# Performance work log

Hardware: AMD Instinct MI355X
Metric: run time of the kernel (lower is better)

## Reference

```python
import jax, jax.numpy as jnp
import numpy as np

nT, nB, H, V = 256, 256, 1024, 32000

def setup_inputs() -> dict:
    key = jax.random.key(0)
    ks = jax.random.split(key, 16)
    s = 0.02
    return {
        "tokens": jax.random.randint(ks[0], (nB,), 0, V),
        "prev_hidden": jax.random.normal(ks[1], (1, nB, H), dtype=jnp.float32),
        "enc_outputs": jax.random.normal(ks[2], (nT, nB, H), dtype=jnp.float32),
        "emb": jax.random.normal(ks[3], (V, H), dtype=jnp.float32) * s,
        "W_i2h": jax.random.normal(ks[4], (H, H), dtype=jnp.float32) * s,
        "W_h2h": jax.random.normal(ks[5], (H, H), dtype=jnp.float32) * s,
        "b_h2h": jnp.zeros((H,), dtype=jnp.float32),
        "w_score": jax.random.normal(ks[6], (H,), dtype=jnp.float32) * s,
        "W_ih": jax.random.normal(ks[7], (3 * H, 2 * H), dtype=jnp.float32) * s,
        "b_ih": jnp.zeros((3 * H,), dtype=jnp.float32),
        "W_hh": jax.random.normal(ks[8], (3 * H, H), dtype=jnp.float32) * s,
        "b_hh": jnp.zeros((3 * H,), dtype=jnp.float32),
        "W_out": jax.random.normal(ks[9], (V, H), dtype=jnp.float32) * s,
        "b_out": jnp.zeros((V,), dtype=jnp.float32),
    }

def reference(tokens, prev_hidden, enc_outputs, emb, W_i2h, W_h2h, b_h2h,
              w_score, W_ih, b_ih, W_hh, b_hh, W_out, b_out):
    h0 = prev_hidden[0]                                     # [nB,H]
    cur_emb = emb[tokens]                                   # [nB,H] (dropout = identity at inference)
    # additive (Bahdanau) attention energies
    enc_proj = jnp.einsum('tbh,oh->tbo', enc_outputs, W_i2h)  # [nT,nB,H]
    h_proj = h0 @ W_h2h.T + b_h2h                           # [nB,H]
    e = jnp.einsum('tbh,h->tb', jnp.tanh(enc_proj + h_proj[None]), w_score)  # [nT,nB]
    alpha = jax.nn.softmax(e.T, axis=1)                     # [nB,nT], softmax over time
    context = jnp.einsum('bt,tbh->bh', alpha, enc_outputs)  # [nB,H]
    x = jnp.concatenate([context, cur_emb], axis=1)         # [nB,2H]
    # single GRU step (PyTorch gate order: r, z, n)
    gi = x @ W_ih.T + b_ih                                  # [nB,3H]
    gh = h0 @ W_hh.T + b_hh                                 # [nB,3H]
    hs = h0.shape[-1]
    r = jax.nn.sigmoid(gi[:, :hs] + gh[:, :hs])
    z = jax.nn.sigmoid(gi[:, hs:2*hs] + gh[:, hs:2*hs])
    n = jnp.tanh(gi[:, 2*hs:] + r * gh[:, 2*hs:])
    h_new = (1.0 - z) * n + z * h0                          # [nB,H]
    out = jax.nn.log_softmax(h_new @ W_out.T + b_out, axis=1)  # [nB,V]
    return out, h_new[None], alpha
```

## Files before the change

### kernel.cpp

```cpp
#include <hip/hip_runtime.h>
#include <hip/hip_bf16.h>

typedef __attribute__((ext_vector_type(8))) short bf16x8;
typedef __attribute__((ext_vector_type(4))) float f32x4;
typedef __attribute__((ext_vector_type(4))) int i32x4;
typedef __attribute__((ext_vector_type(4))) unsigned short u16x4;
typedef __attribute__((ext_vector_type(8))) unsigned short u16x8;

#define LDS_STRIDE 72

__device__ __forceinline__ unsigned short f2bf(float f) {
    __hip_bfloat16 h = __float2bfloat16(f);
    unsigned short u; __builtin_memcpy(&u, &h, 2); return u;
}
__device__ __forceinline__ float bf2f(unsigned short u) {
    union { unsigned u; float f; } v; v.u = ((unsigned)u) << 16; return v.f;
}
__device__ __forceinline__ float fast_sigmoid(float x) { return 1.f / (1.f + __expf(-x)); }
__device__ __forceinline__ float fast_tanh(float x)    { return 1.f - 2.f / (__expf(2.f * x) + 1.f); }

#define GLOAD_LDS16(gp, lp) __builtin_amdgcn_global_load_lds( \
    (const __attribute__((address_space(1))) void*)(gp), \
    (__attribute__((address_space(3))) void*)(lp), 16, 0, 0)


#define STA(LB, HF, PTR) do { \
    GLOAD_LDS16((PTR), &AL[LB][HF][ldsrow][0]); \
    GLOAD_LDS16((PTR) + 65536, &AL[LB][HF][64 + ldsrow][0]); \
} while (0)

#define STB(LB, HF, PTR) do { \
    GLOAD_LDS16((PTR), &BL[LB][HF][ldsrow][0]); \
    GLOAD_LDS16((PTR) + 65536, &BL[LB][HF][64 + ldsrow][0]); \
} while (0)

#define LDA(DST, BUF, MH, KS) do { \
    const int c_ = ((KS)*32 + fg*8) ^ swzr; \
    _Pragma("unroll") \
    for (int mi = 0; mi < 4; ++mi) \
        DST[mi] = *(const bf16x8*)&AL[BUF][wr][(MH)*64 + mi*16 + fr][c_]; \
} while (0)

#define LDB(DST, BUF, KS) do { \
    const int c_ = ((KS)*32 + fg*8) ^ swzr; \
    _Pragma("unroll") \
    for (int ni = 0; ni < 4; ++ni) \
        DST[ni] = *(const bf16x8*)&BL[BUF][bh][br0 + ni*16 + fr][c_]; \
} while (0)

#define MM(AV, BV, MH) do { \
    _Pragma("unroll") \
    for (int mi = 0; mi < 4; ++mi) \
        _Pragma("unroll") \
        for (int ni = 0; ni < 4; ++ni) \
            acc[(MH)*4 + mi][ni] = __builtin_amdgcn_mfma_f32_16x16x32_bf16( \
                AV[mi], BV[ni], acc[(MH)*4 + mi][ni], 0, 0, 0); \
} while (0)

#define SP1 __builtin_amdgcn_s_setprio(1)
#define SP0 __builtin_amdgcn_s_setprio(0)
#define BAR asm volatile("s_barrier" ::: "memory")
#define VMC8 asm volatile("s_waitcnt vmcnt(8)" ::: "memory")
#define VMC0 asm volatile("s_waitcnt vmcnt(0)" ::: "memory")

__global__ __launch_bounds__(512, 1)
void gemm8p_e(const unsigned short* __restrict__ Ag, const unsigned short* __restrict__ Bg,
              const float* __restrict__ hproj, const float* __restrict__ wscore,
              float* __restrict__ epart)
{
    const int tid = threadIdx.x;
    const int lane = tid & 63, wid = tid >> 6;
    const int fr = lane & 15, fg = lane >> 4;
    const int wr = wid >> 2;
    const int wc = wid & 3;
    const int bh = wc >> 1, br0 = (wc & 1) * 64;

    const int cpx = (int)gridDim.x >> 3;
    const int swz = ((int)blockIdx.x & 7) * cpx + ((int)blockIdx.x >> 3);
    const int mb = swz >> 2, nb = swz & 3;
    const int m0 = mb << 8, n0 = nb << 8;

    __shared__ unsigned short AL[3][2][128][64];
    __shared__ unsigned short BL[2][2][128][64];

    const int srow = lane >> 3;
    const int scol = ((lane & 7) ^ srow) << 3;
    const int swzr = (fr & 7) << 3;
    const int ldsrow = wid * 8;

    const unsigned short* pA0 = Ag + (size_t)(m0 + ldsrow + srow) * 1024 + scol;
    const unsigned short* pA1 = pA0 + (size_t)128 * 1024;
    const unsigned short* pB0 = Bg + (size_t)(n0 + ldsrow + srow) * 1024 + scol;
    const unsigned short* pB1 = pB0 + (size_t)128 * 1024;

    f32x4 acc[8][4];
#pragma unroll
    for (int i = 0; i < 8; ++i)
#pragma unroll
        for (int j = 0; j < 4; ++j) acc[i][j] = (f32x4){0.f, 0.f, 0.f, 0.f};
    bf16x8 avA[4], avB[4], bvA[4], bvB[4];

    STA(0, 0, pA0);      STA(0, 1, pA1);
    STB(0, 0, pB0);      STB(0, 1, pB1);
    STA(1, 0, pA0 + 64); STA(1, 1, pA1 + 64);
    STB(1, 0, pB0 + 64); STB(1, 1, pB1 + 64);
    VMC8;
    BAR;

#pragma unroll
    for (int t = 0; t < 16; t += 2) {
        const int tof = t * 64;
        const int a0 = t % 3, a1 = (t + 1) % 3, a2 = (t + 2) % 3, a3 = (t + 3) % 3;
        LDB(bvA, 0, 0); LDA(avA, a0, 0, 0);
        SP1; MM(avA, bvA, 0); SP0;
        LDB(bvB, 0, 1); LDA(avB, a0, 0, 1);
        if (t + 2 < 16) STA(a2, 0, pA0 + tof + 128);
        BAR;
        SP1; MM(avB, bvB, 0); SP0;
        LDA(avA, a0, 1, 0);
        if (t + 2 < 16) STA(a2, 1, pA1 + tof + 128);
        BAR;
        SP1; MM(avA, bvA, 1); SP0;
        LDA(avB, a0, 1, 1);
        if (t + 2 < 16) STB(0, 0, pB0 + tof + 128);
        BAR;
        SP1; MM(avB, bvB, 1); SP0;
        if (t + 2 < 16) { STB(0, 1, pB1 + tof + 128); VMC8; } else { VMC0; }
        BAR;
        LDB(bvA, 1, 0); LDA(avA, a1, 0, 0);
        SP1; MM(avA, bvA, 0); SP0;
        LDB(bvB, 1, 1); LDA(avB, a1, 0, 1);
        if (t + 3 < 16) STA(a3, 0, pA0 + tof + 192);
        BAR;
        SP1; MM(avB, bvB, 0); SP0;
        LDA(avA, a1, 1, 0);
        if (t + 3 < 16) STA(a3, 1, pA1 + tof + 192);
        BAR;
        SP1; MM(avA, bvA, 1); SP0;
        LDA(avB, a1, 1, 1);
        if (t + 3 < 16) STB(1, 0, pB0 + tof + 192);
        BAR;
        SP1; MM(avB, bvB, 1); SP0;
        if (t + 3 < 16) { STB(1, 1, pB1 + tof + 192); VMC8; }
        BAR;
    }

    float wsv[4];
#pragma unroll
    for (int ni = 0; ni < 4; ++ni) wsv[ni] = wscore[n0 + wc * 64 + ni * 16 + fr];
#pragma unroll
    for (int mi = 0; mi < 8; ++mi)
#pragma unroll
        for (int r = 0; r < 4; ++r) {
            const int bb = wr * 128 + mi * 16 + fg * 4 + r;
            const float* hp = hproj + (size_t)bb * 1024 + n0 + wc * 64 + fr;
            float s = 0.f;
#pragma unroll
            for (int ni = 0; ni < 4; ++ni)
                s += fast_tanh(acc[mi][ni][r] + hp[ni * 16]) * wsv[ni];
            s += __shfl_xor(s, 1); s += __shfl_xor(s, 2);
            s += __shfl_xor(s, 4); s += __shfl_xor(s, 8);
            if (fr == 0) epart[((size_t)bb * 256 + mb) * 16 + nb * 4 + wc] = s;
        }
}

__global__ __launch_bounds__(256, 2)
void gemm_h2(const float* __restrict__ h0,
             const float* __restrict__ Wh2h, const float* __restrict__ Whh,
             const float* __restrict__ bh2h, const float* __restrict__ bhh,
             float* __restrict__ hproj, float* __restrict__ gh)
{
    const int mb = blockIdx.x & 1;
    const int nbg = blockIdx.x >> 1;
    const float* Bf; const float* bias; float* Cout; int Nst; int n0;
    if (nbg < 8) { Bf = Wh2h; bias = bh2h; Cout = hproj; Nst = 1024; n0 = nbg << 7; }
    else         { Bf = Whh;  bias = bhh;  Cout = gh;    Nst = 3072; n0 = (nbg - 8) << 7; }

    const int m0 = mb << 7;
    const int tid = threadIdx.x;
    const int lane = tid & 63, wid = tid >> 6;
    const int fr = lane & 15, fg = lane >> 4;
    const int srow = tid >> 1, shalf = (tid & 1) * 32;

    extern __shared__ char smem[];
    typedef unsigned short (*tile_t)[128][LDS_STRIDE];
    tile_t As = (tile_t)smem;
    tile_t Bs = (tile_t)(smem + 2 * 128 * LDS_STRIDE * 2);

    f32x4 acc[2][8];
#pragma unroll
    for (int i = 0; i < 2; ++i)
#pragma unroll
        for (int j = 0; j < 8; ++j) acc[i][j] = (f32x4){0.f, 0.f, 0.f, 0.f};

    float a_f[32], b_f[32];

    auto loadA = [&](int kt) {
        size_t base = (size_t)(m0 + srow) * 1024 + (size_t)kt * 64 + shalf;
#pragma unroll
        for (int j = 0; j < 8; ++j) *(f32x4*)&a_f[j * 4] = *(const f32x4*)(h0 + base + j * 4);
    };
    auto loadB = [&](int kt) {
        size_t base = (size_t)(n0 + srow) * 1024 + (size_t)kt * 64 + shalf;
#pragma unroll
        for (int j = 0; j < 8; ++j) *(f32x4*)&b_f[j * 4] = *(const f32x4*)(Bf + base + j * 4);
    };
    auto storeA = [&](int buf) {
        unsigned short t[32];
#pragma unroll
        for (int j = 0; j < 32; ++j) t[j] = f2bf(a_f[j]);
#pragma unroll
        for (int j = 0; j < 4; ++j) *(i32x4*)&As[buf][srow][shalf + j * 8] = *(i32x4*)&t[j * 8];
    };
    auto storeB = [&](int buf) {
        unsigned short t[32];
#pragma unroll
        for (int j = 0; j < 32; ++j) t[j] = f2bf(b_f[j]);
#pragma unroll
        for (int j = 0; j < 4; ++j) *(i32x4*)&Bs[buf][srow][shalf + j * 8] = *(i32x4*)&t[j * 8];
    };

    loadA(0); loadB(0);
    storeA(0); storeB(0);
    __syncthreads();

    for (int kt = 0; kt < 16; ++kt) {
        const int cur = kt & 1;
        if (kt + 1 < 16) { loadA(kt + 1); loadB(kt + 1); }
#pragma unroll
        for (int ks = 0; ks < 2; ++ks) {
            bf16x8 av[2], bv[8];
#pragma unroll
            for (int mi = 0; mi < 2; ++mi)
                av[mi] = *(const bf16x8*)&As[cur][wid * 32 + mi * 16 + fr][ks * 32 + fg * 8];
#pragma unroll
            for (int ni = 0; ni < 8; ++ni)
                bv[ni] = *(const bf16x8*)&Bs[cur][ni * 16 + fr][ks * 32 + fg * 8];
#pragma unroll
            for (int mi = 0; mi < 2; ++mi)
#pragma unroll
                for (int ni = 0; ni < 8; ++ni)
                    acc[mi][ni] = __builtin_amdgcn_mfma_f32_16x16x32_bf16(av[mi], bv[ni], acc[mi][ni], 0, 0, 0);
        }
        if (kt + 1 < 16) { storeA(cur ^ 1); storeB(cur ^ 1); }
        __syncthreads();
    }

#pragma unroll
    for (int mi = 0; mi < 2; ++mi)
#pragma unroll
        for (int r = 0; r < 4; ++r) {
            const int m = m0 + wid * 32 + mi * 16 + fg * 4 + r;
#pragma unroll
            for (int ni = 0; ni < 8; ++ni) {
                const int col = n0 + ni * 16 + fr;
                Cout[(size_t)m * Nst + col] = acc[mi][ni][r] + bias[col];
            }
        }
}

template<int EPI, bool ABF, bool BBF>
__global__ __launch_bounds__(256, 2)
void gemm_rs(const void* __restrict__ Agv, const void* __restrict__ Bgv,
             const float* __restrict__ bias, float* __restrict__ Cout,
             unsigned short* __restrict__ CoutB,
             const float* __restrict__ hproj, const float* __restrict__ wscore,
             float* __restrict__ epart, float* __restrict__ lsepart,
             int M, int N, int K)
{
    const int nbn = N >> 7;
    const int nmb = M >> 7;
    int mb, nb;
    if (EPI == 1) {
        int cpx = gridDim.x >> 3;
        int bp = (blockIdx.x & 7) * cpx + (blockIdx.x >> 3);
        mb = bp / nbn; nb = bp % nbn;
    } else {
        mb = blockIdx.x % nmb; nb = blockIdx.x / nmb;
    }
    const int m0 = mb << 7, n0 = nb << 7;
    const int tid = threadIdx.x;
    const int lane = tid & 63, wid = tid >> 6;
    const int fr = lane & 15, fg = lane >> 4;
    const int srow = tid >> 1, shalf = (tid & 1) * 32;

    extern __shared__ char smem[];
    typedef unsigned short (*tile_t)[128][LDS_STRIDE];
    tile_t As = (tile_t)smem;
    tile_t Bs = (tile_t)(smem + 2 * 128 * LDS_STRIDE * 2);

    const float* Af = (const float*)Agv;
    const unsigned short* Ab = (const unsigned short*)Agv;
    const float* Bf = (const float*)Bgv;
    const unsigned short* Bb = (const unsigned short*)Bgv;

    f32x4 acc[2][8];
#pragma unroll
    for (int i = 0; i < 2; ++i)
#pragma unroll
        for (int j = 0; j < 8; ++j) acc[i][j] = (f32x4){0.f, 0.f, 0.f, 0.f};

    float a_f[32]; unsigned short a_b[32];
    float b_f[32]; unsigned short b_b[32];

    auto loadA = [&](int kt) {
        size_t base = (size_t)(m0 + srow) * K + (size_t)kt * 64 + shalf;
        if (ABF) {
#pragma unroll
            for (int j = 0; j < 4; ++j) *(i32x4*)&a_b[j * 8] = *(const i32x4*)(Ab + base + j * 8);
        } else {
#pragma unroll
            for (int j = 0; j < 8; ++j) *(f32x4*)&a_f[j * 4] = *(const f32x4*)(Af + base + j * 4);
        }
    };
    auto loadB = [&](int kt) {
        size_t base = (size_t)(n0 + srow) * K + (size_t)kt * 64 + shalf;
        if (BBF) {
#pragma unroll
            for (int j = 0; j < 4; ++j) *(i32x4*)&b_b[j * 8] = *(const i32x4*)(Bb + base + j * 8);
        } else {
#pragma unroll
            for (int j = 0; j < 8; ++j) *(f32x4*)&b_f[j * 4] = *(const f32x4*)(Bf + base + j * 4);
        }
    };
    auto storeA = [&](int buf) {
        unsigned short tA[32];
        if (ABF) {
#pragma unroll
            for (int j = 0; j < 32; ++j) tA[j] = a_b[j];
        } else {
#pragma unroll
            for (int j = 0; j < 32; ++j) tA[j] = f2bf(a_f[j]);
        }
#pragma unroll
        for (int j = 0; j < 4; ++j) *(i32x4*)&As[buf][srow][shalf + j * 8] = *(i32x4*)&tA[j * 8];
    };
    auto storeB = [&](int buf) {
        unsigned short tB[32];
        if (BBF) {
#pragma unroll
            for (int j = 0; j < 32; ++j) tB[j] = b_b[j];
        } else {
#pragma unroll
            for (int j = 0; j < 32; ++j) tB[j] = f2bf(b_f[j]);
        }
#pragma unroll
        for (int j = 0; j < 4; ++j) *(i32x4*)&Bs[buf][srow][shalf + j * 8] = *(i32x4*)&tB[j * 8];
    };

    const int nkt = K >> 6;

    loadA(0); loadB(0);
    storeA(0); storeB(0);
    __syncthreads();

    for (int kt = 0; kt < nkt; ++kt) {
        const int cur = kt & 1;
        if (kt + 1 < nkt) { loadA(kt + 1); loadB(kt + 1); }
#pragma unroll
        for (int ks = 0; ks < 2; ++ks) {
            bf16x8 av[2], bv[8];
#pragma unroll
            for (int mi = 0; mi < 2; ++mi)
                av[mi] = *(const bf16x8*)&As[cur][wid * 32 + mi * 16 + fr][ks * 32 + fg * 8];
#pragma unroll
            for (int ni = 0; ni < 8; ++ni)
                bv[ni] = *(const bf16x8*)&Bs[cur][ni * 16 + fr][ks * 32 + fg * 8];
#pragma unroll
            for (int mi = 0; mi < 2; ++mi)
#pragma unroll
                for (int ni = 0; ni < 8; ++ni)
                    acc[mi][ni] = __builtin_amdgcn_mfma_f32_16x16x32_bf16(av[mi], bv[ni], acc[mi][ni], 0, 0, 0);
        }
        if (kt + 1 < nkt) { storeA(cur ^ 1); storeB(cur ^ 1); }
        __syncthreads();
    }

    if (EPI == 0) {
#pragma unroll
        for (int mi = 0; mi < 2; ++mi)
#pragma unroll
            for (int r = 0; r < 4; ++r) {
                const int m = m0 + wid * 32 + mi * 16 + fg * 4 + r;
#pragma unroll
                for (int ni = 0; ni < 8; ++ni) {
                    const int col = n0 + ni * 16 + fr;
                    Cout[(size_t)m * N + col] = acc[mi][ni][r] + bias[col];
                }
            }
    } else if (EPI == 1) {
        float wsv[8];
#pragma unroll
        for (int ni = 0; ni < 8; ++ni) wsv[ni] = wscore[n0 + ni * 16 + fr];
#pragma unroll
        for (int mi = 0; mi < 2; ++mi)
#pragma unroll
            for (int r = 0; r < 4; ++r) {
                const int m = m0 + wid * 32 + mi * 16 + fg * 4 + r;
                const int bb = m & 255, tt = m >> 8;
                const float* hp = hproj + (size_t)bb * 1024 + n0 + fr;
                float s = 0.f;
#pragma unroll
                for (int ni = 0; ni < 8; ++ni)
                    s += fast_tanh(acc[mi][ni][r] + hp[ni * 16]) * wsv[ni];
                s += __shfl_xor(s, 1); s += __shfl_xor(s, 2);
                s += __shfl_xor(s, 4); s += __shfl_xor(s, 8);
                if (fr == 0) epart[((size_t)bb * 256 + tt) * 8 + nb] = s;
            }
    } else {
#pragma unroll
        for (int mi = 0; mi < 2; ++mi)
#pragma unroll
            for (int r = 0; r < 4; ++r) {
                const int m = m0 + wid * 32 + mi * 16 + fg * 4 + r;
                float vv[8];
                float mx = -3.4e38f;
#pragma unroll
                for (int ni = 0; ni < 8; ++ni) {
                    const int col = n0 + ni * 16 + fr;
                    vv[ni] = acc[mi][ni][r] + bias[col];
                    CoutB[(size_t)m * N + col] = f2bf(vv[ni]);
                    mx = fmaxf(mx, vv[ni]);
                }
                mx = fmaxf(mx, __shfl_xor(mx, 1));
                mx = fmaxf(mx, __shfl_xor(mx, 2));
                mx = fmaxf(mx, __shfl_xor(mx, 4));
                mx = fmaxf(mx, __shfl_xor(mx, 8));
                float se = 0.f;
#pragma unroll
                for (int ni = 0; ni < 8; ++ni) se += __expf(vv[ni] - mx);
                se += __shfl_xor(se, 1); se += __shfl_xor(se, 2);
                se += __shfl_xor(se, 4); se += __shfl_xor(se, 8);
                if (fr == 0) {
                    lsepart[((size_t)m * nbn + nb) * 2]     = mx;
                    lsepart[((size_t)m * nbn + nb) * 2 + 1] = se;
                }
            }
    }
}

__global__ void prep_all(const float* __restrict__ enc, unsigned short* __restrict__ encB,
                         const float* __restrict__ Wi2h, unsigned short* __restrict__ WiB,
                         const float* __restrict__ emb, const int* __restrict__ tokens,
                         unsigned short* __restrict__ xB)
{
    const int ENC4 = 16777216, WI4 = 262144, EMB4 = 65536;
    const int total = ENC4 + WI4 + EMB4;
    for (int i = blockIdx.x * 256 + threadIdx.x; i < total; i += gridDim.x * 256) {
        f32x4 v; unsigned short* dst;
        if (i < ENC4) {
            v = *(const f32x4*)(enc + (size_t)i * 4);
            dst = encB + (size_t)i * 4;
        } else if (i < ENC4 + WI4) {
            int j = i - ENC4;
            v = *(const f32x4*)(Wi2h + (size_t)j * 4);
            dst = WiB + (size_t)j * 4;
        } else {
            int j = i - ENC4 - WI4;
            int b = j >> 8, h4 = j & 255;
            v = *(const f32x4*)(emb + (size_t)tokens[b] * 1024 + h4 * 4);
            dst = xB + (size_t)b * 2048 + 1024 + h4 * 4;
        }
        u16x4 o;
#pragma unroll
        for (int j = 0; j < 4; ++j) o[j] = f2bf(v[j]);
        *(u16x4*)dst = o;
    }
}

__global__ void prep_kernel(const float* __restrict__ Wi2h, unsigned short* __restrict__ WiB,
                            const float* __restrict__ emb, const int* __restrict__ tokens,
                            unsigned short* __restrict__ xB)
{
    int i = blockIdx.x * 256 + threadIdx.x;
    if (i < 262144) {
        f32x4 v = *(const f32x4*)(Wi2h + (size_t)i * 4);
        u16x4 o;
#pragma unroll
        for (int j = 0; j < 4; ++j) o[j] = f2bf(v[j]);
        *(u16x4*)(WiB + (size_t)i * 4) = o;
    } else {
        int j = i - 262144;
        int b = j >> 8, h4 = j & 255;
        int tok = tokens[b];
        f32x4 v = *(const f32x4*)(emb + (size_t)tok * 1024 + h4 * 4);
        u16x4 o;
#pragma unroll
        for (int jj = 0; jj < 4; ++jj) o[jj] = f2bf(v[jj]);
        *(u16x4*)(xB + (size_t)b * 2048 + 1024 + h4 * 4) = o;
    }
}

__global__ __launch_bounds__(256) void softmax_alpha(const float* __restrict__ epart,
                                                     float* __restrict__ alpha, int pw)
{
    const int b = blockIdx.x, t = threadIdx.x;
    const int lane = t & 63, w = t >> 6;
    const float* ep = epart + ((size_t)b * 256 + t) * pw;
    float s = 0.f;
    for (int j = 0; j < pw; ++j) s += ep[j];
    __shared__ float rmax[4], rsum[4];
    float mx = s;
#pragma unroll
    for (int d = 1; d < 64; d <<= 1) mx = fmaxf(mx, __shfl_xor(mx, d));
    if (lane == 0) rmax[w] = mx;
    __syncthreads();
    mx = fmaxf(fmaxf(rmax[0], rmax[1]), fmaxf(rmax[2], rmax[3]));
    float p = __expf(s - mx);
    float sm = p;
#pragma unroll
    for (int d = 1; d < 64; d <<= 1) sm += __shfl_xor(sm, d);
    if (lane == 0) rsum[w] = sm;
    __syncthreads();
    sm = rsum[0] + rsum[1] + rsum[2] + rsum[3];
    alpha[(size_t)b * 256 + t] = p / sm;
}

__global__ __launch_bounds__(128) void ctx_part_bf(const float* __restrict__ alpha,
                                                   const unsigned short* __restrict__ encB,
                                                   float* __restrict__ pc)
{
    const int b = blockIdx.x, tc = blockIdx.y;
    const int h8 = threadIdx.x;
    const float* al = alpha + (size_t)b * 256 + tc * 64;
    float acc[8];
#pragma unroll
    for (int j = 0; j < 8; ++j) acc[j] = 0.f;
#pragma unroll 4
    for (int i = 0; i < 64; ++i) {
        float a = al[i];
        u16x8 e = *(const u16x8*)(encB + ((size_t)(tc * 64 + i) * 256 + b) * 1024 + h8 * 8);
#pragma unroll
        for (int j = 0; j < 8; ++j) acc[j] += bf2f(e[j]) * a;
    }
    float* d = pc + ((size_t)tc * 256 + b) * 1024 + h8 * 8;
    *(f32x4*)d = *(f32x4*)&acc[0];
    *(f32x4*)(d + 4) = *(f32x4*)&acc[4];
}

__global__ __launch_bounds__(256) void ctx_part(const float* __restrict__ alpha,
                                                const float* __restrict__ enc,
                                                float* __restrict__ pc)
{
    const int b = blockIdx.x, tc = blockIdx.y;
    const int h4 = threadIdx.x;
    const float* al = alpha + (size_t)b * 256 + tc * 64;
    f32x4 acc = {0.f, 0.f, 0.f, 0.f};
#pragma unroll 4
    for (int i = 0; i < 64; ++i) {
        float a = al[i];
        f32x4 e = *(const f32x4*)(enc + ((size_t)(tc * 64 + i) * 256 + b) * 1024 + h4 * 4);
        acc += e * a;
    }
    *(f32x4*)(pc + ((size_t)tc * 256 + b) * 1024 + h4 * 4) = acc;
}

__global__ void ctx_fin(const float* __restrict__ pc, unsigned short* __restrict__ xB)
{
    const int b = blockIdx.x, h4 = threadIdx.x;
    f32x4 c = {0.f, 0.f, 0.f, 0.f};
#pragma unroll
    for (int tc = 0; tc < 4; ++tc)
        c += *(const f32x4*)(pc + ((size_t)tc * 256 + b) * 1024 + h4 * 4);
    u16x4 o;
#pragma unroll
    for (int j = 0; j < 4; ++j) o[j] = f2bf(c[j]);
    *(u16x4*)(xB + (size_t)b * 2048 + h4 * 4) = o;
}

__global__ void gru_kernel(const float* __restrict__ gi, const float* __restrict__ gh,
                           const float* __restrict__ h0, float* __restrict__ hnew,
                           unsigned short* __restrict__ hnB)
{
    int idx = blockIdx.x * 256 + threadIdx.x;
    int b = idx >> 10, h = idx & 1023;
    size_t gb = (size_t)b * 3072;
    float r = fast_sigmoid(gi[gb + h]        + gh[gb + h]);
    float z = fast_sigmoid(gi[gb + 1024 + h] + gh[gb + 1024 + h]);
    float n = fast_tanh   (gi[gb + 2048 + h] + r * gh[gb + 2048 + h]);
    float hp = h0[idx];
    float hn = (1.f - z) * n + z * hp;
    hnew[idx] = hn;
    hnB[idx] = f2bf(hn);
}

__global__ void lse_reduce(const float* __restrict__ lsepart, float* __restrict__ lse, int nbn)
{
    const int m = blockIdx.x, l = threadIdx.x;
    float mx = -3.4e38f, s = 0.f;
    for (int p = l; p < nbn; p += 64) {
        float pm = lsepart[((size_t)m * nbn + p) * 2];
        float ps = lsepart[((size_t)m * nbn + p) * 2 + 1];
        float nm = fmaxf(mx, pm);
        s = s * __expf(mx - nm) + ps * __expf(pm - nm);
        mx = nm;
    }
#pragma unroll
    for (int d = 1; d < 64; d <<= 1) {
        float om = __shfl_xor(mx, d), os = __shfl_xor(s, d);
        float nm = fmaxf(mx, om);
        s = s * __expf(mx - nm) + os * __expf(om - nm);
        mx = nm;
    }
    if (l == 0) lse[m] = mx + __logf(s);
}

__global__ void lsub_bf(const unsigned short* __restrict__ lgB,
                        const float* __restrict__ lse, float* __restrict__ out)
{
    int f = blockIdx.x * 256 + threadIdx.x;
    float l = lse[f / 4000];
    u16x8 v = *(const u16x8*)(lgB + (size_t)f * 8);
    float* o = out + (size_t)f * 8;
    f32x4 o0, o1;
#pragma unroll
    for (int j = 0; j < 4; ++j) o0[j] = bf2f(v[j]) - l;
#pragma unroll
    for (int j = 0; j < 4; ++j) o1[j] = bf2f(v[4 + j]) - l;
    *(f32x4*)o = o0;
    *(f32x4*)(o + 4) = o1;
}

extern "C" void kernel_launch(void* const* d_in, const int* in_sizes, int n_in,
                              void* d_out, int out_size, void* d_ws, size_t ws_size,
                              hipStream_t stream)
{
    const int*   tokens  = (const int*)  d_in[0];
    const float* h0      = (const float*)d_in[1];
    const float* enc     = (const float*)d_in[2];
    const float* emb     = (const float*)d_in[3];
    const float* W_i2h   = (const float*)d_in[4];
    const float* W_h2h   = (const float*)d_in[5];
    const float* b_h2h   = (const float*)d_in[6];
    const float* w_score = (const float*)d_in[7];
    const float* W_ih    = (const float*)d_in[8];
    const float* b_ih    = (const float*)d_in[9];
    const float* W_hh    = (const float*)d_in[10];
    const float* b_hh    = (const float*)d_in[11];
    const float* W_out   = (const float*)d_in[12];
    const float* b_out   = (const float*)d_in[13];

    float* out   = (float*)d_out;
    float* hnew  = out + (size_t)256 * 32000;
    float* alpha = hnew + 256 * 1024;

    const size_t RS_LDS = 2u * 2u * 128u * LDS_STRIDE * 2u;

    char* w = (char*)d_ws;
    const size_t NEED = (size_t)153 * (1 << 20);

    if (ws_size >= NEED) {
        unsigned short* encB  = (unsigned short*)(w);
        unsigned short* lgB   = (unsigned short*)(w);
        unsigned short* WiB   = (unsigned short*)(w + (size_t)128 * (1 << 20));
        float* hproj          = (float*)(w + (size_t)130 * (1 << 20));
        float* gh             = (float*)(w + (size_t)131 * (1 << 20));
        float* epart          = (float*)(w + (size_t)134 * (1 << 20));
        float* pc             = (float*)(w + (size_t)138 * (1 << 20));
        unsigned short* xB    = (unsigned short*)(w + (size_t)142 * (1 << 20));
        float* gi             = (float*)(w + (size_t)143 * (1 << 20));
        unsigned short* hnB   = (unsigned short*)(w + (size_t)146 * (1 << 20));
        float* lsepart        = (float*)(w + (size_t)147 * (1 << 20));
        float* lse            = (float*)(w + (size_t)148 * (1 << 20));

        prep_all<<<2048, 256, 0, stream>>>(enc, encB, W_i2h, WiB, emb, tokens, xB);
        gemm_h2<<<64, 256, RS_LDS, stream>>>(h0, W_h2h, W_hh, b_h2h, b_hh, hproj, gh);
        gemm8p_e<<<1024, 512, 0, stream>>>(encB, WiB, hproj, w_score, epart);
        softmax_alpha<<<256, 256, 0, stream>>>(epart, alpha, 16);
        ctx_part_bf<<<dim3(256, 4), 128, 0, stream>>>(alpha, encB, pc);
        ctx_fin<<<256, 256, 0, stream>>>(pc, xB);
        gemm_rs<0, true, false><<<48, 256, RS_LDS, stream>>>(xB, W_ih, b_ih, gi,
            nullptr, nullptr, nullptr, nullptr, nullptr, 256, 3072, 2048);
        gru_kernel<<<1024, 256, 0, stream>>>(gi, gh, h0, hnew, hnB);
        gemm_rs<2, true, false><<<500, 256, RS_LDS, stream>>>(hnB, W_out, b_out, nullptr,
            lgB, nullptr, nullptr, nullptr, lsepart, 256, 32000, 1024);
        lse_reduce<<<256, 64, 0, stream>>>(lsepart, lse, 250);
        lsub_bf<<<4000, 256, 0, stream>>>(lgB, lse, out);
    } else {
        unsigned short* WiB   = (unsigned short*)(w);
        float* hproj          = (float*)(w + (size_t)2  * (1 << 20));
        float* gh             = (float*)(w + (size_t)3  * (1 << 20));
        float* epart          = (float*)(w + (size_t)6  * (1 << 20));
        float* pc             = (float*)(w + (size_t)8  * (1 << 20));
        unsigned short* xB    = (unsigned short*)(w + (size_t)12 * (1 << 20));
        float* gi             = (float*)(w + (size_t)13 * (1 << 20));
        unsigned short* hnB   = (unsigned short*)(w + (size_t)16 * (1 << 20));
        float* lsepart        = (float*)(w + (size_t)17 * (1 << 20));
        float* lse            = (float*)(w + (size_t)18 * (1 << 20));
        unsigned short* lgB   = (unsigned short*)(w + (size_t)19 * (1 << 20));

        prep_kernel<<<1280, 256, 0, stream>>>(W_i2h, WiB, emb, tokens, xB);
        gemm_h2<<<64, 256, RS_LDS, stream>>>(h0, W_h2h, W_hh, b_h2h, b_hh, hproj, gh);
        gemm_rs<1, false, true><<<4096, 256, RS_LDS, stream>>>(enc, WiB, nullptr, nullptr,
            nullptr, hproj, w_score, epart, nullptr, 65536, 1024, 1024);
        softmax_alpha<<<256, 256, 0, stream>>>(epart, alpha, 8);
        ctx_part<<<dim3(256, 4), 256, 0, stream>>>(alpha, enc, pc);
        ctx_fin<<<256, 256, 0, stream>>>(pc, xB);
        gemm_rs<0, true, false><<<48, 256, RS_LDS, stream>>>(xB, W_ih, b_ih, gi,
            nullptr, nullptr, nullptr, nullptr, nullptr, 256, 3072, 2048);
        gru_kernel<<<1024, 256, 0, stream>>>(gi, gh, h0, hnew, hnB);
        gemm_rs<2, true, false><<<500, 256, RS_LDS, stream>>>(hnB, W_out, b_out, nullptr,
            lgB, nullptr, nullptr, nullptr, lsepart, 256, 32000, 1024);
        lse_reduce<<<256, 64, 0, stream>>>(lsepart, lse, 250);
        lsub_bf<<<4000, 256, 0, stream>>>(lgB, lse, out);
    }
}
```

Baseline: 479.3 us.

## Merge prep with h2 GEMM, split-K gi GEMM, fuse LSE reduce and subtract

Folds the h0 projection GEMM into the prep conversion kernel as 64 extra blocks, so both run concurrently in one launch. Replaces the 48-block gi GEMM with a 4-way split-K version (192 blocks) whose partials are summed in a new GRU kernel together with the bias. Fuses the LSE reduction and the log-softmax subtraction into one kernel. The aim is to cut launch count and fill an underoccupied GEMM, at the cost of extra partial-sum traffic and a fused lse_sub kernel that uses only 256 blocks.

```diff
diff --git a/kernel.cpp b/kernel.cpp
--- a/kernel.cpp
+++ b/kernel.cpp
@@ -164,14 +164,13 @@
         }
 }
 
-__global__ __launch_bounds__(256, 2)
-void gemm_h2(const float* __restrict__ h0,
-             const float* __restrict__ Wh2h, const float* __restrict__ Whh,
-             const float* __restrict__ bh2h, const float* __restrict__ bhh,
-             float* __restrict__ hproj, float* __restrict__ gh)
-{
-    const int mb = blockIdx.x & 1;
-    const int nbg = blockIdx.x >> 1;
+__device__ void h2_body(char* smem, int blk, const float* __restrict__ h0,
+                        const float* __restrict__ Wh2h, const float* __restrict__ Whh,
+                        const float* __restrict__ bh2h, const float* __restrict__ bhh,
+                        float* __restrict__ hproj, float* __restrict__ gh)
+{
+    const int mb = blk & 1;
+    const int nbg = blk >> 1;
     const float* Bf; const float* bias; float* Cout; int Nst; int n0;
     if (nbg < 8) { Bf = Wh2h; bias = bh2h; Cout = hproj; Nst = 1024; n0 = nbg << 7; }
     else         { Bf = Whh;  bias = bhh;  Cout = gh;    Nst = 3072; n0 = (nbg - 8) << 7; }
@@ -182,7 +181,6 @@
     const int fr = lane & 15, fg = lane >> 4;
     const int srow = tid >> 1, shalf = (tid & 1) * 32;
 
-    extern __shared__ char smem[];
     typedef unsigned short (*tile_t)[128][LDS_STRIDE];
     tile_t As = (tile_t)smem;
     tile_t Bs = (tile_t)(smem + 2 * 128 * LDS_STRIDE * 2);
@@ -259,194 +257,25 @@
         }
 }
 
-template<int EPI, bool ABF, bool BBF>
 __global__ __launch_bounds__(256, 2)
-void gemm_rs(const void* __restrict__ Agv, const void* __restrict__ Bgv,
-             const float* __restrict__ bias, float* __restrict__ Cout,
-             unsigned short* __restrict__ CoutB,
-             const float* __restrict__ hproj, const float* __restrict__ wscore,
-             float* __restrict__ epart, float* __restrict__ lsepart,
-             int M, int N, int K)
-{
-    const int nbn = N >> 7;
-    const int nmb = M >> 7;
-    int mb, nb;
-    if (EPI == 1) {
-        int cpx = gridDim.x >> 3;
-        int bp = (blockIdx.x & 7) * cpx + (blockIdx.x >> 3);
-        mb = bp / nbn; nb = bp % nbn;
-    } else {
-        mb = blockIdx.x % nmb; nb = blockIdx.x / nmb;
-    }
-    const int m0 = mb << 7, n0 = nb << 7;
-    const int tid = threadIdx.x;
-    const int lane = tid & 63, wid = tid >> 6;
-    const int fr = lane & 15, fg = lane >> 4;
-    const int srow = tid >> 1, shalf = (tid & 1) * 32;
-
+void prep_h2(const float* __restrict__ enc, unsigned short* __restrict__ encB,
+             const float* __restrict__ Wi2h, unsigned short* __restrict__ WiB,
+             const float* __restrict__ emb, const int* __restrict__ tokens,
+             unsigned short* __restrict__ xB,
+             const float* __restrict__ h0,
+             const float* __restrict__ Wh2h, const float* __restrict__ Whh,
+             const float* __restrict__ bh2h, const float* __restrict__ bhh,
+             float* __restrict__ hproj, float* __restrict__ gh)
+{
     extern __shared__ char smem[];
-    typedef unsigned short (*tile_t)[128][LDS_STRIDE];
-    tile_t As = (tile_t)smem;
-    tile_t Bs = (tile_t)(smem + 2 * 128 * LDS_STRIDE * 2);
-
-    const float* Af = (const float*)Agv;
-    const unsigned short* Ab = (const unsigned short*)Agv;
-    const float* Bf = (const float*)Bgv;
-    const unsigned short* Bb = (const unsigned short*)Bgv;
-
-    f32x4 acc[2][8];
-#pragma unroll
-    for (int i = 0; i < 2; ++i)
-#pragma unroll
-        for (int j = 0; j < 8; ++j) acc[i][j] = (f32x4){0.f, 0.f, 0.f, 0.f};
-
-    float a_f[32]; unsigned short a_b[32];
-    float b_f[32]; unsigned short b_b[32];
-
-    auto loadA = [&](int kt) {
-        size_t base = (size_t)(m0 + srow) * K + (size_t)kt * 64 + shalf;
-        if (ABF) {
-#pragma unroll
-            for (int j = 0; j < 4; ++j) *(i32x4*)&a_b[j * 8] = *(const i32x4*)(Ab + base + j * 8);
-        } else {
-#pragma unroll
-            for (int j = 0; j < 8; ++j) *(f32x4*)&a_f[j * 4] = *(const f32x4*)(Af + base + j * 4);
-        }
-    };
-    auto loadB = [&](int kt) {
-        size_t base = (size_t)(n0 + srow) * K + (size_t)kt * 64 + shalf;
-        if (BBF) {
-#pragma unroll
-            for (int j = 0; j < 4; ++j) *(i32x4*)&b_b[j * 8] = *(const i32x4*)(Bb + base + j * 8);
-        } else {
-#pragma unroll
-            for (int j = 0; j < 8; ++j) *(f32x4*)&b_f[j * 4] = *(const f32x4*)(Bf + base + j * 4);
-        }
-    };
-    auto storeA = [&](int buf) {
-        unsigned short tA[32];
-        if (ABF) {
-#pragma unroll
-            for (int j = 0; j < 32; ++j) tA[j] = a_b[j];
-        } else {
-#pragma unroll
-            for (int j = 0; j < 32; ++j) tA[j] = f2bf(a_f[j]);
-        }
-#pragma unroll
-        for (int j = 0; j < 4; ++j) *(i32x4*)&As[buf][srow][shalf + j * 8] = *(i32x4*)&tA[j * 8];
-    };
-    auto storeB = [&](int buf) {
-        unsigned short tB[32];
-        if (BBF) {
-#pragma unroll
-            for (int j = 0; j < 32; ++j) tB[j] = b_b[j];
-        } else {
-#pragma unroll
-            for (int j = 0; j < 32; ++j) tB[j] = f2bf(b_f[j]);
-        }
-#pragma unroll
-        for (int j = 0; j < 4; ++j) *(i32x4*)&Bs[buf][srow][shalf + j * 8] = *(i32x4*)&tB[j * 8];
-    };
-
-    const int nkt = K >> 6;
-
-    loadA(0); loadB(0);
-    storeA(0); storeB(0);
-    __syncthreads();
-
-    for (int kt = 0; kt < nkt; ++kt) {
-        const int cur = kt & 1;
-        if (kt + 1 < nkt) { loadA(kt + 1); loadB(kt + 1); }
-#pragma unroll
-        for (int ks = 0; ks < 2; ++ks) {
-            bf16x8 av[2], bv[8];
-#pragma unroll
-            for (int mi = 0; mi < 2; ++mi)
-                av[mi] = *(const bf16x8*)&As[cur][wid * 32 + mi * 16 + fr][ks * 32 + fg * 8];
-#pragma unroll
-            for (int ni = 0; ni < 8; ++ni)
-                bv[ni] = *(const bf16x8*)&Bs[cur][ni * 16 + fr][ks * 32 + fg * 8];
-#pragma unroll
-            for (int mi = 0; mi < 2; ++mi)
-#pragma unroll
-                for (int ni = 0; ni < 8; ++ni)
-                    acc[mi][ni] = __builtin_amdgcn_mfma_f32_16x16x32_bf16(av[mi], bv[ni], acc[mi][ni], 0, 0, 0);
-        }
-        if (kt + 1 < nkt) { storeA(cur ^ 1); storeB(cur ^ 1); }
-        __syncthreads();
-    }
-
-    if (EPI == 0) {
-#pragma unroll
-        for (int mi = 0; mi < 2; ++mi)
-#pragma unroll
-            for (int r = 0; r < 4; ++r) {
-                const int m = m0 + wid * 32 + mi * 16 + fg * 4 + r;
-#pragma unroll
-                for (int ni = 0; ni < 8; ++ni) {
-                    const int col = n0 + ni * 16 + fr;
-                    Cout[(size_t)m * N + col] = acc[mi][ni][r] + bias[col];
-                }
-            }
-    } else if (EPI == 1) {
-        float wsv[8];
-#pragma unroll
-        for (int ni = 0; ni < 8; ++ni) wsv[ni] = wscore[n0 + ni * 16 + fr];
-#pragma unroll
-        for (int mi = 0; mi < 2; ++mi)
-#pragma unroll
-            for (int r = 0; r < 4; ++r) {
-                const int m = m0 + wid * 32 + mi * 16 + fg * 4 + r;
-                const int bb = m & 255, tt = m >> 8;
-                const float* hp = hproj + (size_t)bb * 1024 + n0 + fr;
-                float s = 0.f;
-#pragma unroll
-                for (int ni = 0; ni < 8; ++ni)
-                    s += fast_tanh(acc[mi][ni][r] + hp[ni * 16]) * wsv[ni];
-                s += __shfl_xor(s, 1); s += __shfl_xor(s, 2);
-                s += __shfl_xor(s, 4); s += __shfl_xor(s, 8);
-                if (fr == 0) epart[((size_t)bb * 256 + tt) * 8 + nb] = s;
-            }
-    } else {
-#pragma unroll
-        for (int mi = 0; mi < 2; ++mi)
-#pragma unroll
-            for (int r = 0; r < 4; ++r) {
-                const int m = m0 + wid * 32 + mi * 16 + fg * 4 + r;
-                float vv[8];
-                float mx = -3.4e38f;
-#pragma unroll
-                for (int ni = 0; ni < 8; ++ni) {
-                    const int col = n0 + ni * 16 + fr;
-                    vv[ni] = acc[mi][ni][r] + bias[col];
-                    CoutB[(size_t)m * N + col] = f2bf(vv[ni]);
-                    mx = fmaxf(mx, vv[ni]);
-                }
-                mx = fmaxf(mx, __shfl_xor(mx, 1));
-                mx = fmaxf(mx, __shfl_xor(mx, 2));
-                mx = fmaxf(mx, __shfl_xor(mx, 4));
-                mx = fmaxf(mx, __shfl_xor(mx, 8));
-                float se = 0.f;
-#pragma unroll
-                for (int ni = 0; ni < 8; ++ni) se += __expf(vv[ni] - mx);
-                se += __shfl_xor(se, 1); se += __shfl_xor(se, 2);
-                se += __shfl_xor(se, 4); se += __shfl_xor(se, 8);
-                if (fr == 0) {
-                    lsepart[((size_t)m * nbn + nb) * 2]     = mx;
-                    lsepart[((size_t)m * nbn + nb) * 2 + 1] = se;
-                }
-            }
-    }
-}
-
-__global__ void prep_all(const float* __restrict__ enc, unsigned short* __restrict__ encB,
-                         const float* __restrict__ Wi2h, unsigned short* __restrict__ WiB,
-                         const float* __restrict__ emb, const int* __restrict__ tokens,
-                         unsigned short* __restrict__ xB)
-{
+    if (blockIdx.x < 64) {
+        h2_body(smem, blockIdx.x, h0, Wh2h, Whh, bh2h, bhh, hproj, gh);
+        return;
+    }
     const int ENC4 = 16777216, WI4 = 262144, EMB4 = 65536;
     const int total = ENC4 + WI4 + EMB4;
-    for (int i = blockIdx.x * 256 + threadIdx.x; i < total; i += gridDim.x * 256) {
+    const int stride = ((int)gridDim.x - 64) * 256;
+    for (int i = ((int)blockIdx.x - 64) * 256 + (int)threadIdx.x; i < total; i += stride) {
         f32x4 v; unsigned short* dst;
         if (i < ENC4) {
             v = *(const f32x4*)(enc + (size_t)i * 4);
@@ -468,6 +297,285 @@
     }
 }
 
+__global__ __launch_bounds__(256, 2)
+void gemm_h2(const float* __restrict__ h0,
+             const float* __restrict__ Wh2h, const float* __restrict__ Whh,
+             const float* __restrict__ bh2h, const float* __restrict__ bhh,
+             float* __restrict__ hproj, float* __restrict__ gh)
+{
+    extern __shared__ char smem[];
+    h2_body(smem, blockIdx.x, h0, Wh2h, Whh, bh2h, bhh, hproj, gh);
+}
+
+__global__ __launch_bounds__(256, 2)
+void gemm_gi(const unsigned short* __restrict__ xB, const float* __restrict__ Wih,
+             float* __restrict__ gip)
+{
+    const int s = blockIdx.x / 48;
+    const int b = blockIdx.x % 48;
+    const int mb = b & 1, nb = b >> 1;
+    const int m0 = mb << 7, n0 = nb << 7;
+    const int kbase = s * 512;
+    const int tid = threadIdx.x;
+    const int lane = tid & 63, wid = tid >> 6;
+    const int fr = lane & 15, fg = lane >> 4;
+    const int srow = tid >> 1, shalf = (tid & 1) * 32;
+
+    extern __shared__ char smem[];
+    typedef unsigned short (*tile_t)[128][LDS_STRIDE];
+    tile_t As = (tile_t)smem;
+    tile_t Bs = (tile_t)(smem + 2 * 128 * LDS_STRIDE * 2);
+
+    f32x4 acc[2][8];
+#pragma unroll
+    for (int i = 0; i < 2; ++i)
+#pragma unroll
+        for (int j = 0; j < 8; ++j) acc[i][j] = (f32x4){0.f, 0.f, 0.f, 0.f};
+
+    unsigned short a_b[32]; float b_f[32];
+
+    auto loadA = [&](int kt) {
+        size_t base = (size_t)(m0 + srow) * 2048 + kbase + (size_t)kt * 64 + shalf;
+#pragma unroll
+        for (int j = 0; j < 4; ++j) *(i32x4*)&a_b[j * 8] = *(const i32x4*)(xB + base + j * 8);
+    };
+    auto loadB = [&](int kt) {
+        size_t base = (size_t)(n0 + srow) * 2048 + kbase + (size_t)kt * 64 + shalf;
+#pragma unroll
+        for (int j = 0; j < 8; ++j) *(f32x4*)&b_f[j * 4] = *(const f32x4*)(Wih + base + j * 4);
+    };
+    auto storeA = [&](int buf) {
+#pragma unroll
+        for (int j = 0; j < 4; ++j) *(i32x4*)&As[buf][srow][shalf + j * 8] = *(i32x4*)&a_b[j * 8];
+    };
+    auto storeB = [&](int buf) {
+        unsigned short t[32];
+#pragma unroll
+        for (int j = 0; j < 32; ++j) t[j] = f2bf(b_f[j]);
+#pragma unroll
+        for (int j = 0; j < 4; ++j) *(i32x4*)&Bs[buf][srow][shalf + j * 8] = *(i32x4*)&t[j * 8];
+    };
+
+    loadA(0); loadB(0);
+    storeA(0); storeB(0);
+    __syncthreads();
+
+    for (int kt = 0; kt < 8; ++kt) {
+        const int cur = kt & 1;
+        if (kt + 1 < 8) { loadA(kt + 1); loadB(kt + 1); }
+#pragma unroll
+        for (int ks = 0; ks < 2; ++ks) {
+            bf16x8 av[2], bv[8];
+#pragma unroll
+            for (int mi = 0; mi < 2; ++mi)
+                av[mi] = *(const bf16x8*)&As[cur][wid * 32 + mi * 16 + fr][ks * 32 + fg * 8];
+#pragma unroll
+            for (int ni = 0; ni < 8; ++ni)
+                bv[ni] = *(const bf16x8*)&Bs[cur][ni * 16 + fr][ks * 32 + fg * 8];
+#pragma unroll
+            for (int mi = 0; mi < 2; ++mi)
+#pragma unroll
+                for (int ni = 0; ni < 8; ++ni)
+                    acc[mi][ni] = __builtin_amdgcn_mfma_f32_16x16x32_bf16(av[mi], bv[ni], acc[mi][ni], 0, 0, 0);
+        }
+        if (kt + 1 < 8) { storeA(cur ^ 1); storeB(cur ^ 1); }
+        __syncthreads();
+    }
+
+    float* Cs = gip + (size_t)s * 256 * 3072;
+#pragma unroll
+    for (int mi = 0; mi < 2; ++mi)
+#pragma unroll
+        for (int r = 0; r < 4; ++r) {
+            const int m = m0 + wid * 32 + mi * 16 + fg * 4 + r;
+#pragma unroll
+            for (int ni = 0; ni < 8; ++ni) {
+                const int col = n0 + ni * 16 + fr;
+                Cs[(size_t)m * 3072 + col] = acc[mi][ni][r];
+            }
+        }
+}
+
+template<int EPI, bool ABF, bool BBF>
+__global__ __launch_bounds__(256, 2)
+void gemm_rs(const void* __restrict__ Agv, const void* __restrict__ Bgv,
+             const float* __restrict__ bias, float* __restrict__ Cout,
+             unsigned short* __restrict__ CoutB,
+             const float* __restrict__ hproj, const float* __restrict__ wscore,
+             float* __restrict__ epart, float* __restrict__ lsepart,
+             int M, int N, int K)
+{
+    const int nbn = N >> 7;
+    const int nmb = M >> 7;
+    int mb, nb;
+    if (EPI == 1) {
+        int cpx = gridDim.x >> 3;
+        int bp = (blockIdx.x & 7) * cpx + (blockIdx.x >> 3);
+        mb = bp / nbn; nb = bp % nbn;
+    } else {
+        mb = blockIdx.x % nmb; nb = blockIdx.x / nmb;
+    }
+    const int m0 = mb << 7, n0 = nb << 7;
+    const int tid = threadIdx.x;
+    const int lane = tid & 63, wid = tid >> 6;
+    const int fr = lane & 15, fg = lane >> 4;
+    const int srow = tid >> 1, shalf = (tid & 1) * 32;
+
+    extern __shared__ char smem[];
+    typedef unsigned short (*tile_t)[128][LDS_STRIDE];
+    tile_t As = (tile_t)smem;
+    tile_t Bs = (tile_t)(smem + 2 * 128 * LDS_STRIDE * 2);
+
+    const float* Af = (const float*)Agv;
+    const unsigned short* Ab = (const unsigned short*)Agv;
+    const float* Bf = (const float*)Bgv;
+    const unsigned short* Bb = (const unsigned short*)Bgv;
+
+    f32x4 acc[2][8];
+#pragma unroll
+    for (int i = 0; i < 2; ++i)
+#pragma unroll
+        for (int j = 0; j < 8; ++j) acc[i][j] = (f32x4){0.f, 0.f, 0.f, 0.f};
+
+    float a_f[32]; unsigned short a_b[32];
+    float b_f[32]; unsigned short b_b[32];
+
+    auto loadA = [&](int kt) {
+        size_t base = (size_t)(m0 + srow) * K + (size_t)kt * 64 + shalf;
+        if (ABF) {
+#pragma unroll
+            for (int j = 0; j < 4; ++j) *(i32x4*)&a_b[j * 8] = *(const i32x4*)(Ab + base + j * 8);
+        } else {
+#pragma unroll
+            for (int j = 0; j < 8; ++j) *(f32x4*)&a_f[j * 4] = *(const f32x4*)(Af + base + j * 4);
+        }
+    };
+    auto loadB = [&](int kt) {
+        size_t base = (size_t)(n0 + srow) * K + (size_t)kt * 64 + shalf;
+        if (BBF) {
+#pragma unroll
+            for (int j = 0; j < 4; ++j) *(i32x4*)&b_b[j * 8] = *(const i32x4*)(Bb + base + j * 8);
+        } else {
+#pragma unroll
+            for (int j = 0; j < 8; ++j) *(f32x4*)&b_f[j * 4] = *(const f32x4*)(Bf + base + j * 4);
+        }
+    };
+    auto storeA = [&](int buf) {
+        unsigned short tA[32];
+        if (ABF) {
+#pragma unroll
+            for (int j = 0; j < 32; ++j) tA[j] = a_b[j];
+        } else {
+#pragma unroll
+            for (int j = 0; j < 32; ++j) tA[j] = f2bf(a_f[j]);
+        }
+#pragma unroll
+        for (int j = 0; j < 4; ++j) *(i32x4*)&As[buf][srow][shalf + j * 8] = *(i32x4*)&tA[j * 8];
+    };
+    auto storeB = [&](int buf) {
+        unsigned short tB[32];
+        if (BBF) {
+#pragma unroll
+            for (int j = 0; j < 32; ++j) tB[j] = b_b[j];
+        } else {
+#pragma unroll
+            for (int j = 0; j < 32; ++j) tB[j] = f2bf(b_f[j]);
+        }
+#pragma unroll
+        for (int j = 0; j < 4; ++j) *(i32x4*)&Bs[buf][srow][shalf + j * 8] = *(i32x4*)&tB[j * 8];
+    };
+
+    const int nkt = K >> 6;
+
+    loadA(0); loadB(0);
+    storeA(0); storeB(0);
+    __syncthreads();
+
+    for (int kt = 0; kt < nkt; ++kt) {
+        const int cur = kt & 1;
+        if (kt + 1 < nkt) { loadA(kt + 1); loadB(kt + 1); }
+#pragma unroll
+        for (int ks = 0; ks < 2; ++ks) {
+            bf16x8 av[2], bv[8];
+#pragma unroll
+            for (int mi = 0; mi < 2; ++mi)
+                av[mi] = *(const bf16x8*)&As[cur][wid * 32 + mi * 16 + fr][ks * 32 + fg * 8];
+#pragma unroll
+            for (int ni = 0; ni < 8; ++ni)
+                bv[ni] = *(const bf16x8*)&Bs[cur][ni * 16 + fr][ks * 32 + fg * 8];
+#pragma unroll
+            for (int mi = 0; mi < 2; ++mi)
+#pragma unroll
+                for (int ni = 0; ni < 8; ++ni)
+                    acc[mi][ni] = __builtin_amdgcn_mfma_f32_16x16x32_bf16(av[mi], bv[ni], acc[mi][ni], 0, 0, 0);
+        }
+        if (kt + 1 < nkt) { storeA(cur ^ 1); storeB(cur ^ 1); }
+        __syncthreads();
+    }
+
+    if (EPI == 0) {
+#pragma unroll
+        for (int mi = 0; mi < 2; ++mi)
+#pragma unroll
+            for (int r = 0; r < 4; ++r) {
+                const int m = m0 + wid * 32 + mi * 16 + fg * 4 + r;
+#pragma unroll
+                for (int ni = 0; ni < 8; ++ni) {
+                    const int col = n0 + ni * 16 + fr;
+                    Cout[(size_t)m * N + col] = acc[mi][ni][r] + bias[col];
+                }
+            }
+    } else if (EPI == 1) {
+        float wsv[8];
+#pragma unroll
+        for (int ni = 0; ni < 8; ++ni) wsv[ni] = wscore[n0 + ni * 16 + fr];
+#pragma unroll
+        for (int mi = 0; mi < 2; ++mi)
+#pragma unroll
+            for (int r = 0; r < 4; ++r) {
+                const int m = m0 + wid * 32 + mi * 16 + fg * 4 + r;
+                const int bb = m & 255, tt = m >> 8;
+                const float* hp = hproj + (size_t)bb * 1024 + n0 + fr;
+                float s = 0.f;
+#pragma unroll
+                for (int ni = 0; ni < 8; ++ni)
+                    s += fast_tanh(acc[mi][ni][r] + hp[ni * 16]) * wsv[ni];
+                s += __shfl_xor(s, 1); s += __shfl_xor(s, 2);
+                s += __shfl_xor(s, 4); s += __shfl_xor(s, 8);
+                if (fr == 0) epart[((size_t)bb * 256 + tt) * 8 + nb] = s;
+            }
+    } else {
+#pragma unroll
+        for (int mi = 0; mi < 2; ++mi)
+#pragma unroll
+            for (int r = 0; r < 4; ++r) {
+                const int m = m0 + wid * 32 + mi * 16 + fg * 4 + r;
+                float vv[8];
+                float mx = -3.4e38f;
+#pragma unroll
+                for (int ni = 0; ni < 8; ++ni) {
+                    const int col = n0 + ni * 16 + fr;
+                    vv[ni] = acc[mi][ni][r] + bias[col];
+                    CoutB[(size_t)m * N + col] = f2bf(vv[ni]);
+                    mx = fmaxf(mx, vv[ni]);
+                }
+                mx = fmaxf(mx, __shfl_xor(mx, 1));
+                mx = fmaxf(mx, __shfl_xor(mx, 2));
+                mx = fmaxf(mx, __shfl_xor(mx, 4));
+                mx = fmaxf(mx, __shfl_xor(mx, 8));
+                float se = 0.f;
+#pragma unroll
+                for (int ni = 0; ni < 8; ++ni) se += __expf(vv[ni] - mx);
+                se += __shfl_xor(se, 1); se += __shfl_xor(se, 2);
+                se += __shfl_xor(se, 4); se += __shfl_xor(se, 8);
+                if (fr == 0) {
+                    lsepart[((size_t)m * nbn + nb) * 2]     = mx;
+                    lsepart[((size_t)m * nbn + nb) * 2 + 1] = se;
+                }
+            }
+    }
+}
+
 __global__ void prep_kernel(const float* __restrict__ Wi2h, unsigned short* __restrict__ WiB,
                             const float* __restrict__ emb, const int* __restrict__ tokens,
                             unsigned short* __restrict__ xB)
@@ -566,6 +674,26 @@
 #pragma unroll
     for (int j = 0; j < 4; ++j) o[j] = f2bf(c[j]);
     *(u16x4*)(xB + (size_t)b * 2048 + h4 * 4) = o;
+}
+
+__global__ void gru4_kernel(const float* __restrict__ gip, const float* __restrict__ gh,
+                            const float* __restrict__ bih, const float* __restrict__ h0,
+                            float* __restrict__ hnew, unsigned short* __restrict__ hnB)
+{
+    int idx = blockIdx.x * 256 + threadIdx.x;
+    int b = idx >> 10, h = idx & 1023;
+    size_t gb = (size_t)b * 3072;
+    const size_t S = (size_t)256 * 3072;
+    float g0 = gip[gb + h]        + gip[S + gb + h]        + gip[2*S + gb + h]        + gip[3*S + gb + h]        + bih[h];
+    float g1 = gip[gb + 1024 + h] + gip[S + gb + 1024 + h] + gip[2*S + gb + 1024 + h] + gip[3*S + gb + 1024 + h] + bih[1024 + h];
+    float g2 = gip[gb + 2048 + h] + gip[S + gb + 2048 + h] + gip[2*S + gb + 2048 + h] + gip[3*S + gb + 2048 + h] + bih[2048 + h];
+    float r = fast_sigmoid(g0 + gh[gb + h]);
+    float z = fast_sigmoid(g1 + gh[gb + 1024 + h]);
+    float n = fast_tanh   (g2 + r * gh[gb + 2048 + h]);
+    float hp = h0[idx];
+    float hn = (1.f - z) * n + z * hp;
+    hnew[idx] = hn;
+    hnB[idx] = f2bf(hn);
 }
 
 __global__ void gru_kernel(const float* __restrict__ gi, const float* __restrict__ gh,
@@ -582,6 +710,49 @@
     float hn = (1.f - z) * n + z * hp;
     hnew[idx] = hn;
     hnB[idx] = f2bf(hn);
+}
+
+__global__ __launch_bounds__(256) void lse_sub(const float* __restrict__ lsepart,
+                                               const unsigned short* __restrict__ lgB,
+                                               float* __restrict__ out)
+{
+    const int m = blockIdx.x, tid = threadIdx.x;
+    const int lane = tid & 63, w = tid >> 6;
+    float mx = -3.4e38f, s = 0.f;
+    if (tid < 250) {
+        mx = lsepart[((size_t)m * 250 + tid) * 2];
+        s  = lsepart[((size_t)m * 250 + tid) * 2 + 1];
+    }
+#pragma unroll
+    for (int d = 1; d < 64; d <<= 1) {
+        float om = __shfl_xor(mx, d), os = __shfl_xor(s, d);
+        float nm = fmaxf(mx, om);
+        s = s * __expf(mx - nm) + os * __expf(om - nm);
+        mx = nm;
+    }
+    __shared__ float smx[4], ssm[4];
+    if (lane == 0) { smx[w] = mx; ssm[w] = s; }
+    __syncthreads();
+    float fm = smx[0], fs = ssm[0];
+#pragma unroll
+    for (int i = 1; i < 4; ++i) {
+        float nm = fmaxf(fm, smx[i]);
+        fs = fs * __expf(fm - nm) + ssm[i] * __expf(smx[i] - nm);
+        fm = nm;
+    }
+    const float lse = fm + __logf(fs);
+    const unsigned short* lrow = lgB + (size_t)m * 32000;
+    float* orow = out + (size_t)m * 32000;
+    for (int j = tid; j < 4000; j += 256) {
+        u16x8 v = *(const u16x8*)(lrow + (size_t)j * 8);
+        f32x4 o0, o1;
+#pragma unroll
+        for (int k = 0; k < 4; ++k) o0[k] = bf2f(v[k]) - lse;
+#pragma unroll
+        for (int k = 0; k < 4; ++k) o1[k] = bf2f(v[4 + k]) - lse;
+        *(f32x4*)(orow + (size_t)j * 8) = o0;
+        *(f32x4*)(orow + (size_t)j * 8 + 4) = o1;
+    }
 }
 
 __global__ void lse_reduce(const float* __restrict__ lsepart, float* __restrict__ lse, int nbn)
@@ -652,30 +823,27 @@
     if (ws_size >= NEED) {
         unsigned short* encB  = (unsigned short*)(w);
         unsigned short* lgB   = (unsigned short*)(w);
+        float* gip            = (float*)(w + (size_t)32 * (1 << 20));
         unsigned short* WiB   = (unsigned short*)(w + (size_t)128 * (1 << 20));
         float* hproj          = (float*)(w + (size_t)130 * (1 << 20));
         float* gh             = (float*)(w + (size_t)131 * (1 << 20));
         float* epart          = (float*)(w + (size_t)134 * (1 << 20));
         float* pc             = (float*)(w + (size_t)138 * (1 << 20));
         unsigned short* xB    = (unsigned short*)(w + (size_t)142 * (1 << 20));
-        float* gi             = (float*)(w + (size_t)143 * (1 << 20));
-        unsigned short* hnB   = (unsigned short*)(w + (size_t)146 * (1 << 20));
-        float* lsepart        = (float*)(w + (size_t)147 * (1 << 20));
-        float* lse            = (float*)(w + (size_t)148 * (1 << 20));
-
-        prep_all<<<2048, 256, 0, stream>>>(enc, encB, W_i2h, WiB, emb, tokens, xB);
-        gemm_h2<<<64, 256, RS_LDS, stream>>>(h0, W_h2h, W_hh, b_h2h, b_hh, hproj, gh);
+        unsigned short* hnB   = (unsigned short*)(w + (size_t)150 * (1 << 20));
+        float* lsepart        = (float*)(w + (size_t)151 * (1 << 20));
+
+        prep_h2<<<2112, 256, RS_LDS, stream>>>(enc, encB, W_i2h, WiB, emb, tokens, xB,
+                                               h0, W_h2h, W_hh, b_h2h, b_hh, hproj, gh);
         gemm8p_e<<<1024, 512, 0, stream>>>(encB, WiB, hproj, w_score, epart);
         softmax_alpha<<<256, 256, 0, stream>>>(epart, alpha, 16);
         ctx_part_bf<<<dim3(256, 4), 128, 0, stream>>>(alpha, encB, pc);
         ctx_fin<<<256, 256, 0, stream>>>(pc, xB);
-        gemm_rs<0, true, false><<<48, 256, RS_LDS, stream>>>(xB, W_ih, b_ih, gi,
-            nullptr, nullptr, nullptr, nullptr, nullptr, 256, 3072, 2048);
-        gru_kernel<<<1024, 256, 0, stream>>>(gi, gh, h0, hnew, hnB);
+        gemm_gi<<<192, 256, RS_LDS, stream>>>(xB, W_ih, gip);
+        gru4_kernel<<<1024, 256, 0, stream>>>(gip, gh, b_ih, h0, hnew, hnB);
         gemm_rs<2, true, false><<<500, 256, RS_LDS, stream>>>(hnB, W_out, b_out, nullptr,
             lgB, nullptr, nullptr, nullptr, lsepart, 256, 32000, 1024);
-        lse_reduce<<<256, 64, 0, stream>>>(lsepart, lse, 250);
-        lsub_bf<<<4000, 256, 0, stream>>>(lgB, lse, out);
+        lse_sub<<<256, 256, 0, stream>>>(lsepart, lgB, out);
     } else {
         unsigned short* WiB   = (unsigned short*)(w);
         float* hproj          = (float*)(w + (size_t)2  * (1 << 20));
```

Result: faster. 415.6 us (-13.3%).
